# Optimization experiments

Measured on AMD Instinct MI355X. Metric: run time of the kernel, lower is better.

The kernel has to match this reference:

```python
import jax, jax.numpy as jnp
import numpy as np
from jax.scipy.ndimage import map_coordinates

IMG = 256
N_ANG = 50
BATCH = 4
N_CNN = 32
IN_CH = 2


def _circle_mask(S):
    c = (S - 1) / 2.0
    yy, xx = jnp.meshgrid(jnp.arange(S, dtype=jnp.float32), jnp.arange(S, dtype=jnp.float32), indexing='ij')
    return (((yy - c) ** 2 + (xx - c) ** 2) <= (S / 2.0) ** 2).astype(jnp.float32)


def radon_forward(img, angles):
    # img [B,1,S,S] -> sinogram [B,1,A,S]; parallel-beam, clip_to_circle=True
    S = img.shape[-1]
    c = (S - 1) / 2.0
    img = img * _circle_mask(S)
    t = jnp.arange(S, dtype=jnp.float32) - c        # integration coord
    s = jnp.arange(S, dtype=jnp.float32) - c        # detector coord
    cos = jnp.cos(angles)[:, None, None]
    sin = jnp.sin(angles)[:, None, None]
    x = s[None, None, :] * cos - t[None, :, None] * sin   # [A,S,S]
    y = s[None, None, :] * sin + t[None, :, None] * cos
    coords = jnp.stack([y + c, x + c])                    # [2,A,S,S] (row, col)
    samp = jax.vmap(lambda im: map_coordinates(im, coords, order=1, mode='constant', cval=0.0))(img[:, 0])  # [B,A,S,S]
    return samp.sum(axis=2)[:, None]                      # sum over ray param -> [B,1,A,S]


def filter_sinogram(sino):
    # Ram-Lak FFT filter with zero-padding + FBP normalization
    S = sino.shape[-1]
    A = sino.shape[2]
    P = max(64, int(2 ** np.ceil(np.log2(2 * S))))
    f = jnp.fft.rfft(jnp.pad(sino, ((0, 0), (0, 0), (0, 0), (0, P - S))), axis=-1)
    ramp = 2.0 * jnp.fft.rfftfreq(P).astype(jnp.float32)
    out = jnp.fft.irfft(f * ramp, n=P, axis=-1)[..., :S]
    return out * (np.pi / (2.0 * A))


def radon_backprojection(sino, angles):
    # sino [B,1,A,S] -> image [B,1,S,S]
    B, _, A, S = sino.shape
    c = (S - 1) / 2.0
    yy, xx = jnp.meshgrid(jnp.arange(S, dtype=jnp.float32) - c, jnp.arange(S, dtype=jnp.float32) - c, indexing='ij')
    cos = jnp.cos(angles)[:, None, None]
    sin = jnp.sin(angles)[:, None, None]
    det = xx[None] * cos + yy[None] * sin + c             # [A,S,S] detector coord
    sino2 = sino[:, 0]                                    # [B,A,S]

    def interp_one(sino_a, idx):
        # sino_a [B,S], idx [S,S] -> [B,S,S] linear interp, zero outside
        i0 = jnp.clip(jnp.floor(idx).astype(jnp.int32), 0, S - 2)
        w = idx - i0
        v = sino_a[:, i0] * (1.0 - w) + sino_a[:, i0 + 1] * w
        valid = (idx >= 0.0) & (idx <= S - 1.0)
        return jnp.where(valid, v, 0.0)

    bp = jax.vmap(interp_one, in_axes=(1, 0))(sino2, det).sum(axis=0)  # [B,S,S]
    return (bp * _circle_mask(S))[:, None]


def conv2d(x, w, b):
    y = jax.lax.conv_general_dilated(x, w, (1, 1), 'SAME', dimension_numbers=('NCHW', 'OIHW', 'NCHW'))
    return y + b[None, :, None, None]


def setup_inputs() -> dict:
    key = jax.random.key(0)
    ks = jax.random.split(key, 10)
    angles = jnp.asarray(np.linspace(0, np.pi, N_ANG, endpoint=False), dtype=jnp.float32)
    return {
        'x_sinogram': jax.random.normal(ks[0], (BATCH, 1, N_ANG, IMG), dtype=jnp.float32),
        'y_img_prev': jax.random.normal(ks[1], (BATCH, 1, IMG, IMG), dtype=jnp.float32),
        'y_img_concat_prev': jax.random.normal(ks[2], (BATCH, 1, IMG, IMG), dtype=jnp.float32),
        'angles': angles,
        'step': jnp.float32(1.0),
        'w1': jax.random.normal(ks[3], (N_CNN, IN_CH, 3, 3), dtype=jnp.float32) * 0.1,
        'b1': jnp.zeros((N_CNN,), dtype=jnp.float32),
        'w2': jax.random.normal(ks[4], (N_CNN, N_CNN, 3, 3), dtype=jnp.float32) * 0.1,
        'b2': jnp.zeros((N_CNN,), dtype=jnp.float32),
        'w3': jax.random.normal(ks[5], (1, N_CNN, 3, 3), dtype=jnp.float32) * 0.1,
        'b3': jnp.zeros((1,), dtype=jnp.float32),
    }


def reference(x_sinogram, y_img_prev, y_img_concat_prev, angles, step, w1, b1, w2, b2, w3, b3):
    Ay = radon_forward(y_img_prev, angles)                 # [B,1,A,S]
    diff = Ay - x_sinogram
    filt = filter_sinogram(diff)
    fbp = radon_backprojection(filt, angles)               # [B,1,S,S]
    y_img_update = y_img_prev + step * fbp
    y_cat = jnp.concatenate([y_img_update, y_img_concat_prev], axis=1)  # [B,2,S,S]
    h = jax.nn.relu(conv2d(y_cat, w1, b1))
    h = jax.nn.relu(conv2d(h, w2, b2))
    y_img = conv2d(h, w3, b3)
    return (y_img, y_img_update)
```

## Files before the change

### kernel.cpp

```cpp
#include <hip/hip_runtime.h>
#include <math.h>

#define IMGS 256
#define NANG 50
#define BATCH 4
#define NCNN 32
#define PIX (IMGS*IMGS)
#define NPIX (BATCH*PIX)

#define OFF_FILT  0
#define OFF_W2BF  51200

static constexpr double PI_D = 3.14159265358979323846;

typedef unsigned short u16;
typedef unsigned int   u32;
typedef unsigned long long u64;
typedef __bf16 bfrag __attribute__((ext_vector_type(8)));
typedef float  ffrag __attribute__((ext_vector_type(4)));

__device__ __forceinline__ u16 f2bf(float f) {
    u32 u = __float_as_uint(f);
    u += 0x7fffu + ((u >> 16) & 1u);
    return (u16)(u >> 16);
}

#define RPITCH_D 131
__global__ __launch_bounds__(1024, 4) void k_A(const float* __restrict__ angles,
                                               const float* __restrict__ yprev,
                                               const float* __restrict__ xsino,
                                               const float* __restrict__ w2,
                                               float* __restrict__ ws) {
    __shared__ u16 limg[258 * 262];
    __shared__ float spart[1024];
    __shared__ float staps[512];
    __shared__ float srow[256];
    int tid = threadIdx.x;
    int gid = blockIdx.x;
    if (gid >= 200) {
        int i = (gid - 200) * 1024 + tid;
        if (i < 9216) {
            int t = i >> 10, oc = (i >> 5) & 31, ic = i & 31;
            ((u16*)(ws + OFF_W2BF))[i] = f2bf(w2[(oc * 32 + ic) * 9 + t]);
        }
        return;
    }
    u32* l32 = (u32*)limg;
    int ra = gid;
    int a = ra % NANG, b = ra / NANG;

    if (tid < 511) {
        int d = tid - 255;
        int n = d < 0 ? -d : d;
        double g;
        if (n == 0) {
            g = 0.5;
        } else {
            double th = PI_D * (double)n / 256.0;
            double S = (256.0 * cos(255.0 * th) - 255.0 * cos(256.0 * th) - 1.0)
                       / (2.0 * (1.0 - cos(th)));
            double sign = (n & 1) ? -1.0 : 1.0;
            g = (sign + S / 128.0) / 512.0;
        }
        staps[tid] = (float)(g * PI_D / 100.0);
    }

    for (int z = tid; z < 772; z += 1024) {
        int addr;
        if (z < 258)      addr = z * RPITCH_D;
        else if (z < 516) addr = (z - 258) * RPITCH_D + 129;
        else if (z < 644) addr = (z - 516) + 1;
        else              addr = 257 * RPITCH_D + (z - 644) + 1;
        l32[addr] = 0;
    }
    const float* __restrict__ src = yprev + b * PIX;
    for (int idx = tid; idx < 16384; idx += 1024) {
        int r = idx >> 6, c4 = (idx & 63) << 2;
        float4 v = *(const float4*)(src + r * 256 + c4);
        float di = (float)r - 127.5f;
        float rr = di * di;
        float d0 = (float)c4 - 127.5f;
        v.x = (rr + d0 * d0 <= 16384.0f) ? v.x : 0.0f;
        v.y = (rr + (d0 + 1.0f) * (d0 + 1.0f) <= 16384.0f) ? v.y : 0.0f;
        v.z = (rr + (d0 + 2.0f) * (d0 + 2.0f) <= 16384.0f) ? v.z : 0.0f;
        v.w = (rr + (d0 + 3.0f) * (d0 + 3.0f) <= 16384.0f) ? v.w : 0.0f;
        u32 p0 = (u32)f2bf(v.x) | ((u32)f2bf(v.y) << 16);
        u32 p1 = (u32)f2bf(v.z) | ((u32)f2bf(v.w) << 16);
        int dw = (r + 1) * RPITCH_D + (c4 >> 1) + 1;
        l32[dw] = p0; l32[dw + 1] = p1;
    }
    __syncthreads();

    float a_ = angles[a];
    float cs = cosf(a_), sn = sinf(a_);
    int lane = tid & 63, w = tid >> 6;
    int s8 = lane & 7, t8 = lane >> 3;
    int sA = w * 16 + s8;
    float scA = (float)sA - 127.5f;

    float loA = (float)(w * 16) - 127.5f, hiA = loA + 7.0f;
    float loB = loA + 8.0f,               hiB = hiA + 8.0f;
    float s2minA = fminf(loA * loA, hiA * hiA);
    float s2maxA = fmaxf(loA * loA, hiA * hiA);
    float s2minB = fminf(loB * loB, hiB * hiB);
    float s2maxB = fmaxf(loB * loB, hiB * hiB);
    float s2min  = fminf(s2minA, s2minB);
    float s2max  = fmaxf(s2maxA, s2maxB);
    float hmax = sqrtf(16770.25f - s2min);
    int j_lo = max(0, (int)ceilf((120.5f - hmax) * 0.125f));
    int j_hi = min(31, (int)floorf((127.5f + hmax) * 0.125f));

    float tc0 = (float)t8 - 127.5f + 8.0f * (float)j_lo;
    float rowA = scA * sn + tc0 * cs + 127.5f;
    float colA = scA * cs - tc0 * sn + 127.5f;
    float rowB = rowA + 8.0f * sn;
    float colB = colA + 8.0f * cs;
    float cs8 = 8.0f * cs, sn8 = 8.0f * sn;
    float accA = 0.0f, accB = 0.0f;
    #pragma unroll 2
    for (int j = j_lo; j <= j_hi; ++j) {
        float t0j = 8.0f * (float)j - 127.5f;
        float t7j = t0j + 7.0f;
        float tmax2 = fmaxf(t0j * t0j, t7j * t7j);
        if (s2max + tmax2 <= 16384.0f) {
            #pragma unroll
            for (int hh = 0; hh < 2; ++hh) {
                float rowv = hh ? rowB : rowA;
                float colv = hh ? colB : colA;
                float fr = floorf(rowv), fc = floorf(colv);
                float wr = rowv - fr, wc = colv - fc;
                int i0 = (int)fr, j0 = (int)fc;
                int ca = j0 + 2;
                int ka = ca >> 1;
                int sh = (ca & 1) << 4;
                int dw = (i0 + 1) * RPITCH_D + ka;
                u32 A = l32[dw],            C = l32[dw + 1];
                u32 B = l32[dw + RPITCH_D], D = l32[dw + RPITCH_D + 1];
                u32 top = (u32)((((u64)C << 32) | (u64)A) >> sh);
                u32 bot = (u32)((((u64)D << 32) | (u64)B) >> sh);
                float tl = __uint_as_float(top << 16);
                float tr_ = __uint_as_float(top & 0xffff0000u);
                float bl = __uint_as_float(bot << 16);
                float br = __uint_as_float(bot & 0xffff0000u);
                float tv = tl + (tr_ - tl) * wc;
                float bv = bl + (br - bl) * wc;
                float sv = tv + (bv - tv) * wr;
                if (hh) accB += sv; else accA += sv;
            }
        } else {
            #pragma unroll
            for (int hh = 0; hh < 2; ++hh) {
                float rowv = hh ? rowB : rowA;
                float colv = hh ? colB : colA;
                float fr = floorf(rowv), fc = floorf(colv);
                float wr = rowv - fr, wc = colv - fc;
                int i0 = (int)fr, j0 = (int)fc;
                bool valid = (rowv > -1.0f) & (rowv < 256.0f) & (colv > -1.0f) & (colv < 256.0f);
                int i0c = min(max(i0, -1), 255);
                int j0c = min(max(j0, -1), 255);
                int ca = j0c + 2;
                int ka = ca >> 1;
                int sh = (ca & 1) << 4;
                int dw = (i0c + 1) * RPITCH_D + ka;
                u32 A = l32[dw],            C = l32[dw + 1];
                u32 B = l32[dw + RPITCH_D], D = l32[dw + RPITCH_D + 1];
                u32 top = (u32)((((u64)C << 32) | (u64)A) >> sh);
                u32 bot = (u32)((((u64)D << 32) | (u64)B) >> sh);
                float tl = __uint_as_float(top << 16);
                float tr_ = __uint_as_float(top & 0xffff0000u);
                float bl = __uint_as_float(bot << 16);
                float br = __uint_as_float(bot & 0xffff0000u);
                float tv = tl + (tr_ - tl) * wc;
                float bv = bl + (br - bl) * wc;
                float sv = tv + (bv - tv) * wr;
                sv = valid ? sv : 0.0f;
                if (hh) accB += sv; else accA += sv;
            }
        }
        rowA += cs8; colA -= sn8; rowB += cs8; colB -= sn8;
    }
    accA += __shfl_xor(accA, 8, 64);
    accA += __shfl_xor(accA, 16, 64);
    accA += __shfl_xor(accA, 32, 64);
    accB += __shfl_xor(accB, 8, 64);
    accB += __shfl_xor(accB, 16, 64);
    accB += __shfl_xor(accB, 32, 64);
    if (t8 == 0) { spart[sA] = accA; spart[sA + 8] = accB; }
    __syncthreads();
    if (tid < 256)
        srow[tid] = spart[tid] - xsino[ra * 256 + tid];
    __syncthreads();
    {
        int s = tid & 255, q = tid >> 8;
        float fa = 0.0f;
        int m0 = q * 64;
        #pragma unroll 8
        for (int m = m0; m < m0 + 64; ++m) fa += srow[m] * staps[s - m + 255];
        spart[tid] = fa;
    }
    __syncthreads();
    if (tid < 256)
        ws[OFF_FILT + ra * 256 + tid] =
            spart[tid] + spart[tid + 256] + spart[tid + 512] + spart[tid + 768];
}

#define H1COLS 82
#define H1PLANE (6*H1COLS*4)
#define H2COLS 80
#define H2PITCH 36
#define SM_H1    0
#define SM_H2    31488
#define SM_SUPD  54528
#define SM_SY2   62848
#define SM_SCS   71168
#define SM_SSN   71368
#define SM_SWP   71568
#define SM_TOTAL 72192

__global__ __launch_bounds__(512, 2) void k_BC(const float* __restrict__ angles,
                                               const float* __restrict__ yprev,
                                               const float* __restrict__ yconc,
                                               const float* __restrict__ stepp,
                                               const float* __restrict__ w1,
                                               const float* __restrict__ b1,
                                               const float* __restrict__ b2,
                                               const float* __restrict__ w3,
                                               const float* __restrict__ b3,
                                               float* __restrict__ ws,
                                               float* __restrict__ dout) {
    __shared__ __align__(16) unsigned char smem[SM_TOTAL];
    float* sf   = (float*)(smem);
    u16*   h1   = (u16*)(smem + SM_H1);
    u16*   sh2  = (u16*)(smem + SM_H2);
    u32*   l32h2= (u32*)(smem + SM_H2);
    float (*supd)[260] = (float(*)[260])(smem + SM_SUPD);
    float (*sy2)[260]  = (float(*)[260])(smem + SM_SY2);
    float* scs = (float*)(smem + SM_SCS);
    float* ssn = (float*)(smem + SM_SSN);
    u32*   swp = (u32*)(smem + SM_SWP);

    int tid = threadIdx.x;
    int b = blockIdx.x >> 7, tile = blockIdx.x & 127;
    int y0 = tile << 1;

    {
        const float4* s4 = (const float4*)(ws + OFF_FILT + b * (NANG * 256));
        float4* d4 = (float4*)sf;
        for (int idx = tid; idx < NANG * 64; idx += 512) d4[idx] = s4[idx];
    }
    if (tid < NANG) {
        float a_ = angles[tid];
        scs[tid] = cosf(a_); ssn[tid] = sinf(a_);
    }
    if (tid < 144) {
        int t = tid >> 4, kd = tid & 15;
        swp[tid] = (u32)f2bf(w3[(2 * kd) * 9 + t]) | ((u32)f2bf(w3[(2 * kd + 1) * 9 + t]) << 16);
    }
    if (tid < 32) {
        int r = tid >> 2, c4 = tid & 3;
        supd[r][(c4 < 2) ? c4 : (c4 + 256)] = 0.0f;
    }
    for (int idx = tid; idx < 8 * 260; idx += 512) {
        int r = idx / 260, c = idx - r * 260;
        int iy = y0 - 3 + r, ix = c - 2;
        sy2[r][c] = ((unsigned)iy < 256u && (unsigned)ix < 256u)
                        ? yconc[b * PIX + iy * 256 + ix] : 0.0f;
    }
    __syncthreads();

    {
        int j = tid & 255, r0 = tid >> 8;
        float xx = (float)j - 127.5f;
        float yyb = (float)(y0 - 3 + r0) - 127.5f;
        float ac0 = 0.f, ac1 = 0.f, ac2 = 0.f, ac3 = 0.f;
        #pragma unroll 2
        for (int a = 0; a < NANG; ++a) {
            float cs = scs[a], sn = ssn[a];
            float d2 = sn + sn;
            float f0 = xx * cs + yyb * sn + 127.5f;
            float f1 = f0 + d2, f2 = f1 + d2, f3 = f2 + d2;
            #define BPSAMP(ff, accv) { \
                float fl = floorf(ff); int i0 = (int)fl; \
                i0 = min(max(i0, 0), 254); \
                float wq = ff - (float)i0; \
                float v = sf[a * 256 + i0] * (1.0f - wq) + sf[a * 256 + i0 + 1] * wq; \
                accv += (ff >= 0.0f && ff <= 255.0f) ? v : 0.0f; }
            BPSAMP(f0, ac0) BPSAMP(f1, ac1) BPSAMP(f2, ac2) BPSAMP(f3, ac3)
            #undef BPSAMP
        }
        float step = stepp[0];
        float accs[4] = {ac0, ac1, ac2, ac3};
        #pragma unroll
        for (int k = 0; k < 4; ++k) {
            int lr = r0 + 2 * k;
            int iy = y0 - 3 + lr;
            float val = 0.0f;
            if ((unsigned)iy < 256u) {
                float yy = (float)iy - 127.5f;
                float mk = (xx * xx + yy * yy <= 16384.0f) ? 1.0f : 0.0f;
                val = yprev[b * PIX + iy * 256 + j] + step * accs[k] * mk;
                if (iy >= y0 && iy <= y0 + 1)
                    dout[NPIX + b * PIX + iy * 256 + j] = val;
            }
            supd[lr][j + 2] = val;
        }
    }
    __syncthreads();

    int wv = tid >> 6, lane = tid & 63;
    int m = lane & 15, quad = lane >> 4;
    float bias0 = b2[m], bias1 = b2[m + 16];
    const u16* __restrict__ w2bf = (const u16*)(ws + OFF_W2BF);

    #pragma unroll 1
    for (int xq = 0; xq < 4; ++xq) {
        int xbase = xq * 64;
        {
            int oc0 = wv * 4;
            float W[72];
            const float4* wsrc = (const float4*)(w1 + oc0 * 18);
            #pragma unroll
            for (int i = 0; i < 18; ++i) ((float4*)W)[i] = wsrc[i];
            float bb0 = b1[oc0], bb1 = b1[oc0 + 1], bb2 = b1[oc0 + 2], bb3 = b1[oc0 + 3];
            u16* hp = h1 + wv * H1PLANE;
            #pragma unroll
            for (int it = 0; it < 4; ++it) {
                int idx = it * 64 + lane;
                if (idx < 246) {
                    int lr = idx / 41, pp = idx - lr * 41;
                    int P = xbase - 9 + 2 * pp;
                    int ir = y0 - 2 + lr;
                    int cgb = P + 1;
                    cgb = min(max(cgb, 0), 256);
                    float a00 = bb0, a01 = bb1, a02 = bb2, a03 = bb3;
                    float a10 = bb0, a11 = bb1, a12 = bb2, a13 = bb3;
                    #pragma unroll
                    for (int ky = 0; ky < 3; ++ky) {
                        float2 ua = *(const float2*)&supd[lr + ky][cgb];
                        float2 ub = *(const float2*)&supd[lr + ky][cgb + 2];
                        float2 ca = *(const float2*)&sy2[lr + ky][cgb];
                        float2 cb2 = *(const float2*)&sy2[lr + ky][cgb + 2];
                        float u[4]  = {ua.x, ua.y, ub.x, ub.y};
                        float c6[4] = {ca.x, ca.y, cb2.x, cb2.y};
                        #pragma unroll
                        for (int kx = 0; kx < 3; ++kx) {
                            int t = ky * 3 + kx;
                            float u0 = u[kx],     c0 = c6[kx];
                            float u1 = u[kx + 1], c1 = c6[kx + 1];
                            a00 += u0 * W[t]      + c0 * W[9 + t];
                            a01 += u0 * W[18 + t] + c0 * W[27 + t];
                            a02 += u0 * W[36 + t] + c0 * W[45 + t];
                            a03 += u0 * W[54 + t] + c0 * W[63 + t];
                            a10 += u1 * W[t]      + c1 * W[9 + t];
                            a11 += u1 * W[18 + t] + c1 * W[27 + t];
                            a12 += u1 * W[36 + t] + c1 * W[45 + t];
                            a13 += u1 * W[54 + t] + c1 * W[63 + t];
                        }
                    }
                    bool rowOK = (unsigned)ir < 256u;
                    bool v0 = rowOK && ((unsigned)P < 256u);
                    bool v1 = rowOK && ((unsigned)(P + 1) < 256u);
                    u32 q00 = 0, q01 = 0, q10 = 0, q11 = 0;
                    if (v0) {
                        q00 = (u32)f2bf(fmaxf(a00, 0.f)) | ((u32)f2bf(fmaxf(a01, 0.f)) << 16);
                        q01 = (u32)f2bf(fmaxf(a02, 0.f)) | ((u32)f2bf(fmaxf(a03, 0.f)) << 16);
                    }
                    if (v1) {
                        q10 = (u32)f2bf(fmaxf(a10, 0.f)) | ((u32)f2bf(fmaxf(a11, 0.f)) << 16);
                        q11 = (u32)f2bf(fmaxf(a12, 0.f)) | ((u32)f2bf(fmaxf(a13, 0.f)) << 16);
                    }
                    uint4* op = (uint4*)(hp + (lr * H1COLS + 2 * pp) * 4);
                    *op = make_uint4(q00, q01, q10, q11);
                }
            }
        }
        __syncthreads();

        {
            bfrag Bf[9][2];
            #pragma unroll
            for (int t = 0; t < 9; ++t) {
                const u16* wp = w2bf + t * 1024 + m * 32 + quad * 8;
                Bf[t][0] = *(const bfrag*)(wp);
                Bf[t][1] = *(const bfrag*)(wp + 16 * 32);
            }
            #pragma unroll
            for (int k = 0; k < 3; ++k) {
                int tl = wv + (k << 3);
                if (tl < 20) {
                    int ridx = tl / 5, pt = tl - ridx * 5;
                    int hy = y0 - 1 + ridx;
                    bool hyOK = (unsigned)hy < 256u;
                    int Lb = 16 * pt + m;
                    const u16* qp = h1 + quad * (2 * H1PLANE);
                    #define LDF(row, L, dst) { \
                        const u16* p0_ = qp + ((row) * H1COLS + (L)) * 4; \
                        uint2 lo_ = *(const uint2*)p0_; \
                        uint2 hi_ = *(const uint2*)(p0_ + H1PLANE); \
                        ((uint2*)&dst)[0] = lo_; ((uint2*)&dst)[1] = hi_; }
                    bfrag A0[3], A1[3];
                    #pragma unroll
                    for (int tx = 0; tx < 3; ++tx) LDF(ridx + 0, Lb + tx, A0[tx])
                    #pragma unroll
                    for (int tx = 0; tx < 3; ++tx) LDF(ridx + 1, Lb + tx, A1[tx])
                    ffrag c0 = {0.f, 0.f, 0.f, 0.f}, c1 = {0.f, 0.f, 0.f, 0.f};
                    #pragma unroll
                    for (int tx = 0; tx < 3; ++tx) {
                        c0 = __builtin_amdgcn_mfma_f32_16x16x32_bf16(A0[tx], Bf[tx][0], c0, 0, 0, 0);
                        c1 = __builtin_amdgcn_mfma_f32_16x16x32_bf16(A0[tx], Bf[tx][1], c1, 0, 0, 0);
                    }
                    #pragma unroll
                    for (int tx = 0; tx < 3; ++tx) LDF(ridx + 2, Lb + tx, A0[tx])
                    #pragma unroll
                    for (int tx = 0; tx < 3; ++tx) {
                        c0 = __builtin_amdgcn_mfma_f32_16x16x32_bf16(A1[tx], Bf[3 + tx][0], c0, 0, 0, 0);
                        c1 = __builtin_amdgcn_mfma_f32_16x16x32_bf16(A1[tx], Bf[3 + tx][1], c1, 0, 0, 0);
                    }
                    #pragma unroll
                    for (int tx = 0; tx < 3; ++tx) {
                        c0 = __builtin_amdgcn_mfma_f32_16x16x32_bf16(A0[tx], Bf[6 + tx][0], c0, 0, 0, 0);
                        c1 = __builtin_amdgcn_mfma_f32_16x16x32_bf16(A0[tx], Bf[6 + tx][1], c1, 0, 0, 0);
                    }
                    #undef LDF
                    #pragma unroll
                    for (int r = 0; r < 4; ++r) {
                        int pl = 16 * pt + quad * 4 + r;
                        int pimg = xbase - 8 + pl;
                        bool ok = hyOK && ((unsigned)pimg < 256u);
                        float f0 = ok ? fmaxf(c0[r] + bias0, 0.0f) : 0.0f;
                        float f1 = ok ? fmaxf(c1[r] + bias1, 0.0f) : 0.0f;
                        u16* op = sh2 + (ridx * H2COLS + pl) * H2PITCH;
                        op[m]      = f2bf(f0);
                        op[m + 16] = f2bf(f1);
                    }
                }
            }
        }
        __syncthreads();

        {
            int px_q = tid >> 2, g = tid & 3;
            int xl = px_q & 63, rr = px_q >> 6;
            int oy = y0 + rr;
            float acc = (g == 0) ? b3[0] : 0.0f;
            #pragma unroll
            for (int ky = 0; ky < 3; ++ky) {
                #pragma unroll
                for (int cx = 0; cx < 3; ++cx) {
                    int t = ky * 3 + cx;
                    int pl = xl + cx + 7;
                    const uint2* q2 = (const uint2*)(l32h2 + ((rr + ky) * H2COLS + pl) * 18 + g * 4);
                    const uint2* wp = (const uint2*)(swp + t * 16 + g * 4);
                    uint2 h0 = q2[0], h1v = q2[1];
                    uint2 w0 = wp[0], w1v = wp[1];
                    acc += __uint_as_float(h0.x << 16) * __uint_as_float(w0.x << 16)
                         + __uint_as_float(h0.x & 0xffff0000u) * __uint_as_float(w0.x & 0xffff0000u)
                         + __uint_as_float(h0.y << 16) * __uint_as_float(w0.y << 16)
                         + __uint_as_float(h0.y & 0xffff0000u) * __uint_as_float(w0.y & 0xffff0000u)
                         + __uint_as_float(h1v.x << 16) * __uint_as_float(w1v.x << 16)
                         + __uint_as_float(h1v.x & 0xffff0000u) * __uint_as_float(w1v.x & 0xffff0000u)
                         + __uint_as_float(h1v.y << 16) * __uint_as_float(w1v.y << 16)
                         + __uint_as_float(h1v.y & 0xffff0000u) * __uint_as_float(w1v.y & 0xffff0000u);
                }
            }
            acc += __shfl_xor(acc, 1, 64);
            acc += __shfl_xor(acc, 2, 64);
            if (g == 0)
                dout[b * PIX + oy * 256 + xbase + xl] = acc;
        }
    }
}

extern "C" void kernel_launch(void* const* d_in, const int* in_sizes, int n_in,
                              void* d_out, int out_size, void* d_ws, size_t ws_size,
                              hipStream_t stream) {
    const float* xsino  = (const float*)d_in[0];
    const float* yprev  = (const float*)d_in[1];
    const float* yconc  = (const float*)d_in[2];
    const float* angles = (const float*)d_in[3];
    const float* stepp  = (const float*)d_in[4];
    const float* w1 = (const float*)d_in[5];
    const float* b1 = (const float*)d_in[6];
    const float* w2 = (const float*)d_in[7];
    const float* b2 = (const float*)d_in[8];
    const float* w3 = (const float*)d_in[9];
    const float* b3 = (const float*)d_in[10];
    float* out = (float*)d_out;
    float* ws  = (float*)d_ws;

    k_A<<<209, 1024, 0, stream>>>(angles, yprev, xsino, w2, ws);
    k_BC<<<BATCH * 128, 512, 0, stream>>>(angles, yprev, yconc, stepp, w1, b1,
                                          b2, w3, b3, ws, out);
}
```

Before: 184.1 us.

## Enlarge fused backprojection+CNN tile from 2 to 4 output rows per block

Each block of the fused backprojection/conv kernel now produces 4 output rows instead of 2. This cuts the halo recomputation of backprojection, conv1 and conv2 rows relative to useful output, and halves the grid to 256 blocks. Shared memory grows to about 98KB and launch bounds drop to one block per CU. The final 1-channel conv now uses one thread per pixel over all 32 channels, with half the threads idle, replacing the 4-way split and shuffle reduction. The risk is lower occupancy and a 256-block grid that underfills the GPU's CUs.

After: 169.5 us. 7.9% less time.

```diff
diff --git a/kernel.cpp b/kernel.cpp
--- a/kernel.cpp
+++ b/kernel.cpp
@@ -204,20 +204,22 @@
             spart[tid] + spart[tid + 256] + spart[tid + 512] + spart[tid + 768];
 }
 
+#define H1ROWS 8
 #define H1COLS 82
-#define H1PLANE (6*H1COLS*4)
+#define H1PLANE (H1ROWS*H1COLS*4)
+#define H2ROWS 6
 #define H2COLS 80
 #define H2PITCH 36
 #define SM_H1    0
-#define SM_H2    31488
-#define SM_SUPD  54528
-#define SM_SY2   62848
-#define SM_SCS   71168
-#define SM_SSN   71368
-#define SM_SWP   71568
-#define SM_TOTAL 72192
-
-__global__ __launch_bounds__(512, 2) void k_BC(const float* __restrict__ angles,
+#define SM_H2    41984
+#define SM_SUPD  76544
+#define SM_SY2   86944
+#define SM_SCS   97344
+#define SM_SSN   97544
+#define SM_SWP   97744
+#define SM_TOTAL 98320
+
+__global__ __launch_bounds__(512, 1) void k_BC(const float* __restrict__ angles,
                                                const float* __restrict__ yprev,
                                                const float* __restrict__ yconc,
                                                const float* __restrict__ stepp,
@@ -240,8 +242,8 @@
     u32*   swp = (u32*)(smem + SM_SWP);
 
     int tid = threadIdx.x;
-    int b = blockIdx.x >> 7, tile = blockIdx.x & 127;
-    int y0 = tile << 1;
+    int b = blockIdx.x >> 6, tile = blockIdx.x & 63;
+    int y0 = tile << 2;
 
     {
         const float4* s4 = (const float4*)(ws + OFF_FILT + b * (NANG * 256));
@@ -256,11 +258,11 @@
         int t = tid >> 4, kd = tid & 15;
         swp[tid] = (u32)f2bf(w3[(2 * kd) * 9 + t]) | ((u32)f2bf(w3[(2 * kd + 1) * 9 + t]) << 16);
     }
-    if (tid < 32) {
+    if (tid < 40) {
         int r = tid >> 2, c4 = tid & 3;
         supd[r][(c4 < 2) ? c4 : (c4 + 256)] = 0.0f;
     }
-    for (int idx = tid; idx < 8 * 260; idx += 512) {
+    for (int idx = tid; idx < 10 * 260; idx += 512) {
         int r = idx / 260, c = idx - r * 260;
         int iy = y0 - 3 + r, ix = c - 2;
         sy2[r][c] = ((unsigned)iy < 256u && (unsigned)ix < 256u)
@@ -272,26 +274,26 @@
         int j = tid & 255, r0 = tid >> 8;
         float xx = (float)j - 127.5f;
         float yyb = (float)(y0 - 3 + r0) - 127.5f;
-        float ac0 = 0.f, ac1 = 0.f, ac2 = 0.f, ac3 = 0.f;
+        float ac0 = 0.f, ac1 = 0.f, ac2 = 0.f, ac3 = 0.f, ac4 = 0.f;
         #pragma unroll 2
         for (int a = 0; a < NANG; ++a) {
             float cs = scs[a], sn = ssn[a];
             float d2 = sn + sn;
             float f0 = xx * cs + yyb * sn + 127.5f;
-            float f1 = f0 + d2, f2 = f1 + d2, f3 = f2 + d2;
+            float f1 = f0 + d2, f2 = f1 + d2, f3 = f2 + d2, f4 = f3 + d2;
             #define BPSAMP(ff, accv) { \
                 float fl = floorf(ff); int i0 = (int)fl; \
                 i0 = min(max(i0, 0), 254); \
                 float wq = ff - (float)i0; \
                 float v = sf[a * 256 + i0] * (1.0f - wq) + sf[a * 256 + i0 + 1] * wq; \
                 accv += (ff >= 0.0f && ff <= 255.0f) ? v : 0.0f; }
-            BPSAMP(f0, ac0) BPSAMP(f1, ac1) BPSAMP(f2, ac2) BPSAMP(f3, ac3)
+            BPSAMP(f0, ac0) BPSAMP(f1, ac1) BPSAMP(f2, ac2) BPSAMP(f3, ac3) BPSAMP(f4, ac4)
             #undef BPSAMP
         }
         float step = stepp[0];
-        float accs[4] = {ac0, ac1, ac2, ac3};
+        float accs[5] = {ac0, ac1, ac2, ac3, ac4};
         #pragma unroll
-        for (int k = 0; k < 4; ++k) {
+        for (int k = 0; k < 5; ++k) {
             int lr = r0 + 2 * k;
             int iy = y0 - 3 + lr;
             float val = 0.0f;
@@ -299,7 +301,7 @@
                 float yy = (float)iy - 127.5f;
                 float mk = (xx * xx + yy * yy <= 16384.0f) ? 1.0f : 0.0f;
                 val = yprev[b * PIX + iy * 256 + j] + step * accs[k] * mk;
-                if (iy >= y0 && iy <= y0 + 1)
+                if ((unsigned)(iy - y0) < 4u)
                     dout[NPIX + b * PIX + iy * 256 + j] = val;
             }
             supd[lr][j + 2] = val;
@@ -324,9 +326,9 @@
             float bb0 = b1[oc0], bb1 = b1[oc0 + 1], bb2 = b1[oc0 + 2], bb3 = b1[oc0 + 3];
             u16* hp = h1 + wv * H1PLANE;
             #pragma unroll
-            for (int it = 0; it < 4; ++it) {
+            for (int it = 0; it < 6; ++it) {
                 int idx = it * 64 + lane;
-                if (idx < 246) {
+                if (idx < 328) {
                     int lr = idx / 41, pp = idx - lr * 41;
                     int P = xbase - 9 + 2 * pp;
                     int ir = y0 - 2 + lr;
@@ -385,9 +387,9 @@
                 Bf[t][1] = *(const bfrag*)(wp + 16 * 32);
             }
             #pragma unroll
-            for (int k = 0; k < 3; ++k) {
+            for (int k = 0; k < 4; ++k) {
                 int tl = wv + (k << 3);
-                if (tl < 20) {
+                if (tl < 30) {
                     int ridx = tl / 5, pt = tl - ridx * 5;
                     int hy = y0 - 1 + ridx;
                     bool hyOK = (unsigned)hy < 256u;
@@ -438,35 +440,29 @@
         }
         __syncthreads();
 
-        {
-            int px_q = tid >> 2, g = tid & 3;
-            int xl = px_q & 63, rr = px_q >> 6;
+        if (tid < 256) {
+            int rr = tid >> 6, xl = tid & 63;
             int oy = y0 + rr;
-            float acc = (g == 0) ? b3[0] : 0.0f;
+            float acc = b3[0];
             #pragma unroll
             for (int ky = 0; ky < 3; ++ky) {
                 #pragma unroll
                 for (int cx = 0; cx < 3; ++cx) {
                     int t = ky * 3 + cx;
-                    int pl = xl + cx + 7;
-                    const uint2* q2 = (const uint2*)(l32h2 + ((rr + ky) * H2COLS + pl) * 18 + g * 4);
-                    const uint2* wp = (const uint2*)(swp + t * 16 + g * 4);
-                    uint2 h0 = q2[0], h1v = q2[1];
-                    uint2 w0 = wp[0], w1v = wp[1];
-                    acc += __uint_as_float(h0.x << 16) * __uint_as_float(w0.x << 16)
-                         + __uint_as_float(h0.x & 0xffff0000u) * __uint_as_float(w0.x & 0xffff0000u)
-                         + __uint_as_float(h0.y << 16) * __uint_as_float(w0.y << 16)
-                         + __uint_as_float(h0.y & 0xffff0000u) * __uint_as_float(w0.y & 0xffff0000u)
-                         + __uint_as_float(h1v.x << 16) * __uint_as_float(w1v.x << 16)
-                         + __uint_as_float(h1v.x & 0xffff0000u) * __uint_as_float(w1v.x & 0xffff0000u)
-                         + __uint_as_float(h1v.y << 16) * __uint_as_float(w1v.y << 16)
-                         + __uint_as_float(h1v.y & 0xffff0000u) * __uint_as_float(w1v.y & 0xffff0000u);
+                    const uint2* q2 = (const uint2*)(l32h2 + ((rr + ky) * H2COLS + xl + cx + 7) * 18);
+                    const uint2* wp = (const uint2*)(swp + t * 16);
+                    #pragma unroll
+                    for (int kd = 0; kd < 8; ++kd) {
+                        uint2 hv = q2[kd];
+                        uint2 wvv = wp[kd];
+                        acc += __uint_as_float(hv.x << 16) * __uint_as_float(wvv.x << 16)
+                             + __uint_as_float(hv.x & 0xffff0000u) * __uint_as_float(wvv.x & 0xffff0000u)
+                             + __uint_as_float(hv.y << 16) * __uint_as_float(wvv.y << 16)
+                             + __uint_as_float(hv.y & 0xffff0000u) * __uint_as_float(wvv.y & 0xffff0000u);
+                    }
                 }
             }
-            acc += __shfl_xor(acc, 1, 64);
-            acc += __shfl_xor(acc, 2, 64);
-            if (g == 0)
-                dout[b * PIX + oy * 256 + xbase + xl] = acc;
+            dout[b * PIX + oy * 256 + xbase + xl] = acc;
         }
     }
 }
@@ -489,6 +485,6 @@
     float* ws  = (float*)d_ws;
 
     k_A<<<209, 1024, 0, stream>>>(angles, yprev, xsino, w2, ws);
-    k_BC<<<BATCH * 128, 512, 0, stream>>>(angles, yprev, yconc, stepp, w1, b1,
-                                          b2, w3, b3, ws, out);
+    k_BC<<<BATCH * 64, 512, 0, stream>>>(angles, yprev, yconc, stepp, w1, b1,
+                                         b2, w3, b3, ws, out);
 }
```
